# Kernel optimization log

Hardware: AMD Instinct MI355X
Metric: run time of the kernel (lower is better)

## Reference

```python
import jax, jax.numpy as jnp
import numpy as np

N = 50000
E = 600000
D = 128


def _mlp(x, W1, b1, W2, b2):
    # Linear -> GELU(exact, matches torch nn.GELU default) -> (Dropout=eval no-op) -> Linear
    h = jax.nn.gelu(x @ W1 + b1, approximate=False)
    return h @ W2 + b2


def setup_inputs() -> dict:
    key = jax.random.key(0)
    ks = jax.random.split(key, 12)
    s = 1.0 / np.sqrt(D)
    inp = {
        "x": jax.random.normal(ks[0], (N, D), dtype=jnp.float32),
        "edge_index": jax.random.randint(ks[1], (2, E), 0, N, dtype=jnp.int64),
        "edge_attr": jax.random.normal(ks[2], (E, D), dtype=jnp.float32),
        # edge_mlp params
        "We1": jax.random.uniform(ks[3], (D, D), jnp.float32, -s, s),
        "be1": jax.random.uniform(ks[4], (D,), jnp.float32, -s, s),
        "We2": jax.random.uniform(ks[5], (D, D), jnp.float32, -s, s),
        "be2": jax.random.uniform(ks[6], (D,), jnp.float32, -s, s),
        # update_mlp params
        "Wu1": jax.random.uniform(ks[7], (D, D), jnp.float32, -s, s),
        "bu1": jax.random.uniform(ks[8], (D,), jnp.float32, -s, s),
        "Wu2": jax.random.uniform(ks[9], (D, D), jnp.float32, -s, s),
        "bu2": jax.random.uniform(ks[10], (D,), jnp.float32, -s, s),
        "eps": jnp.zeros((1,), dtype=jnp.float32),
    }
    return inp


def reference(x, edge_index, edge_attr, We1, be1, We2, be2, Wu1, bu1, Wu2, bu2, eps):
    src, dst = edge_index[0], edge_index[1]
    # gather + fuse + edge MLP: [E, D]
    messages = _mlp(x[src] + edge_attr, We1, be1, We2, be2)
    # scatter-add back to nodes: [N, D]
    aggregated = jax.ops.segment_sum(messages, dst, num_segments=x.shape[0])
    return _mlp((1.0 + eps) * x + aggregated, Wu1, bu1, Wu2, bu2)
```

## Files before the change

### kernel.cpp

```cpp
#include <hip/hip_runtime.h>
#include <hip/hip_bf16.h>

#define ND 128
#define LDA 136

typedef _Float16 f16x8 __attribute__((ext_vector_type(8)));
typedef _Float16 f16x4 __attribute__((ext_vector_type(4)));
typedef float    f32x4 __attribute__((ext_vector_type(4)));

__device__ __forceinline__ float gelu_exact(float v) {
    return 0.5f * v * (1.0f + erff(v * 0.70710678118654752f));
}

__global__ void prep_weights(const float* __restrict__ w0, const float* __restrict__ w1,
                             const float* __restrict__ w2, const float* __restrict__ w3,
                             _Float16* __restrict__ wt) {
    int id = blockIdx.x * blockDim.x + threadIdx.x;
    int m   = id >> 14;
    int idx = id & 16383;
    int c = idx >> 7, k = idx & 127;
    const float* W = (m == 0) ? w0 : (m == 1) ? w1 : (m == 2) ? w2 : w3;
    wt[(m << 14) + (c << 7) + k] = (_Float16)W[(k << 7) + c];
}

template<bool EDGE>
__global__ __launch_bounds__(512, 4) void mlp_fused(
    const float* __restrict__ xp,
    const float* __restrict__ rowin,
    const int*   __restrict__ srcp,
    const int*   __restrict__ dstp,
    const _Float16* __restrict__ wt1,
    const _Float16* __restrict__ wt2,
    const float* __restrict__ b1p,
    const float* __restrict__ b2p,
    const float* __restrict__ epsp,
    float* __restrict__ outp,
    int nRows, int nTiles)
{
    __shared__ _Float16 Abuf[64 * LDA];
    __shared__ _Float16 Hbuf[64 * LDA];

    const int tid  = threadIdx.x;
    const int lane = tid & 63;
    const int wid  = tid >> 6;
    const int wr   = wid >> 2;
    const int wc   = wid & 3;
    const int l15  = lane & 15;
    const int khi  = lane >> 4;

    f16x8 wf1[2][4];
    #pragma unroll
    for (int ct = 0; ct < 2; ++ct) {
        int col = wc * 32 + ct * 16 + l15;
        #pragma unroll
        for (int kk = 0; kk < 4; ++kk)
            wf1[ct][kk] = *(const f16x8*)(wt1 + col * ND + kk * 32 + khi * 8);
    }

    float scale = 1.0f;
    if (!EDGE) scale = 1.0f + epsp[0];

    const int sr = tid >> 3;
    const int sc = (tid & 7) * 4;

    for (int tile = blockIdx.x; tile < nTiles; tile += gridDim.x) {
        const int base = tile * 64;

        {
            int grow = base + sr;
            if (grow < nRows) {
                const float* er = rowin + (size_t)grow * ND;
                const float* xr;
                if (EDGE) xr = xp + (size_t)srcp[grow] * ND;
                else      xr = xp + (size_t)grow * ND;
                #pragma unroll
                for (int i = 0; i < 4; ++i) {
                    int c = sc + i * 32;
                    float4 a = *(const float4*)(er + c);
                    float4 b = *(const float4*)(xr + c);
                    f16x4 v;
                    if (EDGE) {
                        v[0] = (_Float16)(a.x + b.x); v[1] = (_Float16)(a.y + b.y);
                        v[2] = (_Float16)(a.z + b.z); v[3] = (_Float16)(a.w + b.w);
                    } else {
                        v[0] = (_Float16)(a.x + scale * b.x); v[1] = (_Float16)(a.y + scale * b.y);
                        v[2] = (_Float16)(a.z + scale * b.z); v[3] = (_Float16)(a.w + scale * b.w);
                    }
                    *(f16x4*)&Abuf[sr * LDA + c] = v;
                }
            } else {
                #pragma unroll
                for (int i = 0; i < 4; ++i) {
                    f16x4 z = {};
                    *(f16x4*)&Abuf[sr * LDA + sc + i * 32] = z;
                }
            }
        }

        f16x8 wf2[2][4];
        #pragma unroll
        for (int ct = 0; ct < 2; ++ct) {
            int col = wc * 32 + ct * 16 + l15;
            #pragma unroll
            for (int kk = 0; kk < 4; ++kk)
                wf2[ct][kk] = *(const f16x8*)(wt2 + col * ND + kk * 32 + khi * 8);
        }

        __syncthreads();

        f32x4 acc[2][2];
        #pragma unroll
        for (int rt = 0; rt < 2; ++rt)
            #pragma unroll
            for (int ct = 0; ct < 2; ++ct)
                acc[rt][ct] = (f32x4)0.0f;

        #pragma unroll
        for (int kk = 0; kk < 4; ++kk) {
            f16x8 af[2];
            #pragma unroll
            for (int rt = 0; rt < 2; ++rt)
                af[rt] = *(const f16x8*)&Abuf[(wr * 32 + rt * 16 + l15) * LDA + kk * 32 + khi * 8];
            #pragma unroll
            for (int rt = 0; rt < 2; ++rt)
                #pragma unroll
                for (int ct = 0; ct < 2; ++ct)
                    acc[rt][ct] = __builtin_amdgcn_mfma_f32_16x16x32_f16(
                        af[rt], wf1[ct][kk], acc[rt][ct], 0, 0, 0);
        }

        #pragma unroll
        for (int rt = 0; rt < 2; ++rt)
            #pragma unroll
            for (int ct = 0; ct < 2; ++ct) {
                int col = wc * 32 + ct * 16 + l15;
                float bb = b1p[col];
                #pragma unroll
                for (int q = 0; q < 4; ++q) {
                    int rl = wr * 32 + rt * 16 + khi * 4 + q;
                    Hbuf[rl * LDA + col] = (_Float16)gelu_exact(acc[rt][ct][q] + bb);
                }
            }

        __syncthreads();

        f32x4 acc2[2][2];
        #pragma unroll
        for (int rt = 0; rt < 2; ++rt)
            #pragma unroll
            for (int ct = 0; ct < 2; ++ct)
                acc2[rt][ct] = (f32x4)0.0f;

        #pragma unroll
        for (int kk = 0; kk < 4; ++kk) {
            f16x8 hf[2];
            #pragma unroll
            for (int rt = 0; rt < 2; ++rt)
                hf[rt] = *(const f16x8*)&Hbuf[(wr * 32 + rt * 16 + l15) * LDA + kk * 32 + khi * 8];
            #pragma unroll
            for (int rt = 0; rt < 2; ++rt)
                #pragma unroll
                for (int ct = 0; ct < 2; ++ct)
                    acc2[rt][ct] = __builtin_amdgcn_mfma_f32_16x16x32_f16(
                        hf[rt], wf2[ct][kk], acc2[rt][ct], 0, 0, 0);
        }

        #pragma unroll
        for (int rt = 0; rt < 2; ++rt)
            #pragma unroll
            for (int ct = 0; ct < 2; ++ct) {
                int col = wc * 32 + ct * 16 + l15;
                float bb = b2p[col];
                #pragma unroll
                for (int q = 0; q < 4; ++q) {
                    int rl = wr * 32 + rt * 16 + khi * 4 + q;
                    int grow = base + rl;
                    if (grow < nRows) {
                        float v = acc2[rt][ct][q] + bb;
                        if (EDGE) {
                            int d = dstp[grow];
                            atomicAdd(outp + (size_t)d * ND + col, v);
                        } else {
                            outp[(size_t)grow * ND + col] = v;
                        }
                    }
                }
            }
    }
}

extern "C" void kernel_launch(void* const* d_in, const int* in_sizes, int n_in,
                              void* d_out, int out_size, void* d_ws, size_t ws_size,
                              hipStream_t stream)
{
    const float* x   = (const float*)d_in[0];
    const int*   ei  = (const int*)d_in[1];
    const float* ea  = (const float*)d_in[2];
    const float* We1 = (const float*)d_in[3];
    const float* be1 = (const float*)d_in[4];
    const float* We2 = (const float*)d_in[5];
    const float* be2 = (const float*)d_in[6];
    const float* Wu1 = (const float*)d_in[7];
    const float* bu1 = (const float*)d_in[8];
    const float* Wu2 = (const float*)d_in[9];
    const float* bu2 = (const float*)d_in[10];
    const float* eps = (const float*)d_in[11];

    const int E  = in_sizes[1] / 2;
    const int Nn = in_sizes[0] / ND;

    float*    agg = (float*)d_ws;
    _Float16* wt  = (_Float16*)((char*)d_ws + (size_t)Nn * ND * sizeof(float));

    hipMemsetAsync(agg, 0, (size_t)Nn * ND * sizeof(float), stream);

    prep_weights<<<dim3(256), dim3(256), 0, stream>>>(We1, We2, Wu1, Wu2, wt);

    const int tilesE = (E + 63) / 64;
    mlp_fused<true><<<dim3(512), dim3(512), 0, stream>>>(
        x, ea, ei, ei + E, wt, wt + 16384, be1, be2, nullptr,
        agg, E, tilesE);

    const int tilesN = (Nn + 63) / 64;
    mlp_fused<false><<<dim3(512), dim3(512), 0, stream>>>(
        x, agg, nullptr, nullptr, wt + 2 * 16384, wt + 3 * 16384, bu1, bu2, eps,
        (float*)d_out, Nn, tilesN);
}
```

Measured before the change: 675.2 us.

## Sort edges by destination and pre-reduce messages in LDS before atomics

```diff
diff --git a/kernel.cpp b/kernel.cpp
--- a/kernel.cpp
+++ b/kernel.cpp
@@ -3,6 +3,7 @@
 
 #define ND 128
 #define LDA 136
+#define LDM 130
 
 typedef _Float16 f16x8 __attribute__((ext_vector_type(8)));
 typedef _Float16 f16x4 __attribute__((ext_vector_type(4)));
@@ -23,12 +24,57 @@
     wt[(m << 14) + (c << 7) + k] = (_Float16)W[(k << 7) + c];
 }
 
-template<bool EDGE>
+__global__ void hist_kernel(const int* __restrict__ dst, int* __restrict__ cnt, int E) {
+    int e = blockIdx.x * blockDim.x + threadIdx.x;
+    if (e < E) atomicAdd(&cnt[dst[e]], 1);
+}
+
+__global__ void scan_exclusive(int* __restrict__ data, int n) {
+    __shared__ int wsum[16];
+    __shared__ int carry;
+    const int t = threadIdx.x, lane = t & 63, wv = t >> 6;
+    if (t == 0) carry = 0;
+    __syncthreads();
+    for (int base = 0; base < n; base += 1024) {
+        int i = base + t;
+        int v = (i < n) ? data[i] : 0;
+        int s = v;
+        #pragma unroll
+        for (int off = 1; off < 64; off <<= 1) {
+            int u = __shfl_up(s, off, 64);
+            if (lane >= off) s += u;
+        }
+        if (lane == 63) wsum[wv] = s;
+        __syncthreads();
+        if (t == 0) {
+            int run = carry;
+            #pragma unroll
+            for (int w = 0; w < 16; ++w) { int x = wsum[w]; wsum[w] = run; run += x; }
+            carry = run;
+        }
+        __syncthreads();
+        int excl = s - v + wsum[wv];
+        if (i < n) data[i] = excl;
+        __syncthreads();
+    }
+}
+
+__global__ void scatter_kernel(const int* __restrict__ dst, int* __restrict__ cur,
+                               int* __restrict__ perm, int E) {
+    int e = blockIdx.x * blockDim.x + threadIdx.x;
+    if (e < E) {
+        int p = atomicAdd(&cur[dst[e]], 1);
+        perm[p] = e;
+    }
+}
+
+template<bool EDGE, bool SORTED>
 __global__ __launch_bounds__(512, 4) void mlp_fused(
     const float* __restrict__ xp,
     const float* __restrict__ rowin,
     const int*   __restrict__ srcp,
     const int*   __restrict__ dstp,
+    const int*   __restrict__ permp,
     const _Float16* __restrict__ wt1,
     const _Float16* __restrict__ wt2,
     const float* __restrict__ b1p,
@@ -37,8 +83,11 @@
     float* __restrict__ outp,
     int nRows, int nTiles)
 {
-    __shared__ _Float16 Abuf[64 * LDA];
-    __shared__ _Float16 Hbuf[64 * LDA];
+    __shared__ __align__(16) char lds_raw[64 * LDA * 2 * sizeof(_Float16)];
+    __shared__ int dtile[64];
+    _Float16* Abuf = (_Float16*)lds_raw;
+    _Float16* Hbuf = (_Float16*)(lds_raw + 64 * LDA * sizeof(_Float16));
+    float*    Mbuf = (float*)lds_raw;
 
     const int tid  = threadIdx.x;
     const int lane = tid & 63;
@@ -48,13 +97,18 @@
     const int l15  = lane & 15;
     const int khi  = lane >> 4;
 
-    f16x8 wf1[2][4];
+    f16x8 wf1[2][4], wf2[2][4];
+    float bb1[2], bb2[2];
     #pragma unroll
     for (int ct = 0; ct < 2; ++ct) {
         int col = wc * 32 + ct * 16 + l15;
         #pragma unroll
-        for (int kk = 0; kk < 4; ++kk)
+        for (int kk = 0; kk < 4; ++kk) {
             wf1[ct][kk] = *(const f16x8*)(wt1 + col * ND + kk * 32 + khi * 8);
+            wf2[ct][kk] = *(const f16x8*)(wt2 + col * ND + kk * 32 + khi * 8);
+        }
+        bb1[ct] = b1p[col];
+        bb2[ct] = b2p[col];
     }
 
     float scale = 1.0f;
@@ -69,9 +123,12 @@
         {
             int grow = base + sr;
             if (grow < nRows) {
-                const float* er = rowin + (size_t)grow * ND;
+                int prow = grow;
+                if (EDGE && SORTED) prow = permp[grow];
+                if (EDGE && SORTED && (tid & 7) == 0) dtile[sr] = dstp[prow];
+                const float* er = rowin + (size_t)prow * ND;
                 const float* xr;
-                if (EDGE) xr = xp + (size_t)srcp[grow] * ND;
+                if (EDGE) xr = xp + (size_t)srcp[prow] * ND;
                 else      xr = xp + (size_t)grow * ND;
                 #pragma unroll
                 for (int i = 0; i < 4; ++i) {
@@ -89,6 +146,7 @@
                     *(f16x4*)&Abuf[sr * LDA + c] = v;
                 }
             } else {
+                if (EDGE && SORTED && (tid & 7) == 0) dtile[sr] = -1;
                 #pragma unroll
                 for (int i = 0; i < 4; ++i) {
                     f16x4 z = {};
@@ -97,15 +155,6 @@
             }
         }
 
-        f16x8 wf2[2][4];
-        #pragma unroll
-        for (int ct = 0; ct < 2; ++ct) {
-            int col = wc * 32 + ct * 16 + l15;
-            #pragma unroll
-            for (int kk = 0; kk < 4; ++kk)
-                wf2[ct][kk] = *(const f16x8*)(wt2 + col * ND + kk * 32 + khi * 8);
-        }
-
         __syncthreads();
 
         f32x4 acc[2][2];
@@ -134,11 +183,10 @@
             #pragma unroll
             for (int ct = 0; ct < 2; ++ct) {
                 int col = wc * 32 + ct * 16 + l15;
-                float bb = b1p[col];
                 #pragma unroll
                 for (int q = 0; q < 4; ++q) {
                     int rl = wr * 32 + rt * 16 + khi * 4 + q;
-                    Hbuf[rl * LDA + col] = (_Float16)gelu_exact(acc[rt][ct][q] + bb);
+                    Hbuf[rl * LDA + col] = (_Float16)gelu_exact(acc[rt][ct][q] + bb1[ct]);
                 }
             }
 
@@ -165,27 +213,61 @@
                         hf[rt], wf2[ct][kk], acc2[rt][ct], 0, 0, 0);
         }
 
-        #pragma unroll
-        for (int rt = 0; rt < 2; ++rt)
-            #pragma unroll
-            for (int ct = 0; ct < 2; ++ct) {
-                int col = wc * 32 + ct * 16 + l15;
-                float bb = b2p[col];
-                #pragma unroll
-                for (int q = 0; q < 4; ++q) {
-                    int rl = wr * 32 + rt * 16 + khi * 4 + q;
-                    int grow = base + rl;
-                    if (grow < nRows) {
-                        float v = acc2[rt][ct][q] + bb;
-                        if (EDGE) {
-                            int d = dstp[grow];
-                            atomicAdd(outp + (size_t)d * ND + col, v);
-                        } else {
-                            outp[(size_t)grow * ND + col] = v;
+        if (EDGE && SORTED) {
+            __syncthreads();
+
+            #pragma unroll
+            for (int rt = 0; rt < 2; ++rt)
+                #pragma unroll
+                for (int ct = 0; ct < 2; ++ct) {
+                    int col = wc * 32 + ct * 16 + l15;
+                    #pragma unroll
+                    for (int q = 0; q < 4; ++q) {
+                        int rl = wr * 32 + rt * 16 + khi * 4 + q;
+                        Mbuf[rl * LDM + col] = acc2[rt][ct][q] + bb2[ct];
+                    }
+                }
+
+            __syncthreads();
+
+            const int rc = tid & 127;
+            const int rg = tid >> 7;
+            float a = 0.0f;
+            #pragma unroll
+            for (int r = rg * 16; r < rg * 16 + 16; ++r) {
+                int d = dtile[r];
+                if (d >= 0) {
+                    a += Mbuf[r * LDM + rc];
+                    if (r == 63 || r == rg * 16 + 15 || dtile[r + 1] != d) {
+                        atomicAdd(outp + (size_t)d * ND + rc, a);
+                        a = 0.0f;
+                    }
+                }
+            }
+
+            __syncthreads();
+        } else {
+            #pragma unroll
+            for (int rt = 0; rt < 2; ++rt)
+                #pragma unroll
+                for (int ct = 0; ct < 2; ++ct) {
+                    int col = wc * 32 + ct * 16 + l15;
+                    #pragma unroll
+                    for (int q = 0; q < 4; ++q) {
+                        int rl = wr * 32 + rt * 16 + khi * 4 + q;
+                        int grow = base + rl;
+                        if (grow < nRows) {
+                            float v = acc2[rt][ct][q] + bb2[ct];
+                            if (EDGE) {
+                                int d = dstp[grow];
+                                atomicAdd(outp + (size_t)d * ND + col, v);
+                            } else {
+                                outp[(size_t)grow * ND + col] = v;
+                            }
                         }
                     }
                 }
-            }
+        }
     }
 }
 
@@ -209,20 +291,47 @@
     const int E  = in_sizes[1] / 2;
     const int Nn = in_sizes[0] / ND;
 
-    float*    agg = (float*)d_ws;
-    _Float16* wt  = (_Float16*)((char*)d_ws + (size_t)Nn * ND * sizeof(float));
-
-    hipMemsetAsync(agg, 0, (size_t)Nn * ND * sizeof(float), stream);
-
-    prep_weights<<<dim3(256), dim3(256), 0, stream>>>(We1, We2, Wu1, Wu2, wt);
-
+    const size_t aggB = (size_t)Nn * ND * sizeof(float);
+    const size_t cntB = ((size_t)Nn * sizeof(int) + 255) & ~(size_t)255;
+    const size_t prmB = (size_t)E * sizeof(int);
+    const size_t wtB  = 4 * 16384 * sizeof(_Float16);
+    const bool sorted = (ws_size >= aggB + cntB + prmB + wtB);
+
+    float* agg = (float*)d_ws;
     const int tilesE = (E + 63) / 64;
-    mlp_fused<true><<<dim3(512), dim3(512), 0, stream>>>(
-        x, ea, ei, ei + E, wt, wt + 16384, be1, be2, nullptr,
-        agg, E, tilesE);
-
     const int tilesN = (Nn + 63) / 64;
-    mlp_fused<false><<<dim3(512), dim3(512), 0, stream>>>(
-        x, agg, nullptr, nullptr, wt + 2 * 16384, wt + 3 * 16384, bu1, bu2, eps,
-        (float*)d_out, Nn, tilesN);
-}
+
+    if (sorted) {
+        int*      cnt  = (int*)((char*)d_ws + aggB);
+        int*      perm = (int*)((char*)d_ws + aggB + cntB);
+        _Float16* wt   = (_Float16*)((char*)d_ws + aggB + cntB + prmB);
+
+        hipMemsetAsync(d_ws, 0, aggB + cntB, stream);
+        prep_weights<<<dim3(256), dim3(256), 0, stream>>>(We1, We2, Wu1, Wu2, wt);
+
+        const int gE = (E + 511) / 512;
+        hist_kernel<<<dim3(gE), dim3(512), 0, stream>>>(ei + E, cnt, E);
+        scan_exclusive<<<dim3(1), dim3(1024), 0, stream>>>(cnt, Nn);
+        scatter_kernel<<<dim3(gE), dim3(512), 0, stream>>>(ei + E, cnt, perm, E);
+
+        mlp_fused<true, true><<<dim3(512), dim3(512), 0, stream>>>(
+            x, ea, ei, ei + E, perm, wt, wt + 16384, be1, be2, nullptr,
+            agg, E, tilesE);
+
+        mlp_fused<false, false><<<dim3(512), dim3(512), 0, stream>>>(
+            x, agg, nullptr, nullptr, nullptr, wt + 2 * 16384, wt + 3 * 16384,
+            bu1, bu2, eps, (float*)d_out, Nn, tilesN);
+    } else {
+        _Float16* wt = (_Float16*)((char*)d_ws + aggB);
+        hipMemsetAsync(agg, 0, aggB, stream);
+        prep_weights<<<dim3(256), dim3(256), 0, stream>>>(We1, We2, Wu1, Wu2, wt);
+
+        mlp_fused<true, false><<<dim3(512), dim3(512), 0, stream>>>(
+            x, ea, ei, ei + E, nullptr, wt, wt + 16384, be1, be2, nullptr,
+            agg, E, tilesE);
+
+        mlp_fused<false, false><<<dim3(512), dim3(512), 0, stream>>>(
+            x, agg, nullptr, nullptr, nullptr, wt + 2 * 16384, wt + 3 * 16384,
+            bu1, bu2, eps, (float*)d_out, Nn, tilesN);
+    }
+}
```

After: 631.5 us. 6.5% less time.
